# Kernel tuning notes

Measured on AMD Instinct MI355X. Metric: run time of the kernel, lower is better.

Reference implementation:

```python
import jax, jax.numpy as jnp
import numpy as np

B, S, F_IN = 8, 2048, 1024
H, SC = 512, 256
N_LAYERS = 3


def _glorot(key, shape):
    fan_in, fan_out = shape[-2], shape[-1]
    lim = float(np.sqrt(6.0 / (fan_in + fan_out)))
    return jax.random.uniform(key, shape, jnp.float32, -lim, lim)


def setup_inputs() -> dict:
    key = jax.random.key(0)
    ks = jax.random.split(key, 8)
    x = jax.random.normal(ks[0], (B, S, F_IN), jnp.float32)
    Wp = _glorot(ks[1], (F_IN, H)); bp = jnp.zeros((H,), jnp.float32)
    gcn_W = _glorot(ks[2], (N_LAYERS, H, H)); gcn_b = jnp.zeros((N_LAYERS, H), jnp.float32)
    s1_W = _glorot(ks[3], (H, SC)); s1_b = jnp.zeros((SC,), jnp.float32)
    s2_W = _glorot(ks[4], (SC, SC // 2)); s2_b = jnp.zeros((SC // 2,), jnp.float32)
    s3_W = _glorot(ks[5], (SC // 2, 1)); s3_b = jnp.zeros((1,), jnp.float32)
    return {"x": x, "Wp": Wp, "bp": bp, "gcn_W": gcn_W, "gcn_b": gcn_b,
            "s1_W": s1_W, "s1_b": s1_b, "s2_W": s2_W, "s2_b": s2_b,
            "s3_W": s3_W, "s3_b": s3_b}


def _build_adj(seq_len):
    # tridiagonal band: self + immediate temporal neighbors
    a = jnp.eye(seq_len, dtype=jnp.float32)
    a = a + jnp.eye(seq_len, k=1, dtype=jnp.float32) + jnp.eye(seq_len, k=-1, dtype=jnp.float32)
    deg = a.sum(axis=1)
    dinv = jnp.power(deg + 1e-8, -0.5)
    # D^{-1/2} A D^{-1/2}
    return dinv[:, None] * a * dinv[None, :]


def reference(x, Wp, bp, gcn_W, gcn_b, s1_W, s1_b, s2_W, s2_b, s3_W, s3_b):
    seq_len = x.shape[1]
    adj = _build_adj(seq_len)  # [S, S]
    h = jnp.einsum('bsf,fh->bsh', x, Wp) + bp  # feature projection
    for i in range(N_LAYERS):
        support = jnp.einsum('bsh,hk->bsk', h, gcn_W[i])
        h = jnp.einsum('st,btk->bsk', adj, support) + gcn_b[i]
        if i < N_LAYERS - 1:
            h = jax.nn.relu(h)  # dropout is identity in eval mode
    z = jax.nn.relu(jnp.einsum('bsh,hc->bsc', h, s1_W) + s1_b)
    z = jax.nn.relu(jnp.einsum('bsc,cd->bsd', z, s2_W) + s2_b)
    scores = jax.nn.sigmoid(jnp.einsum('bsd,do->bso', z, s3_W) + s3_b)
    return scores[..., 0]  # [B, S]
```

## Files before the change

### kernel.cpp

```cpp
#include <hip/hip_runtime.h>
#include <hip/hip_fp16.h>
#include <cstdint>
#include <cstddef>


typedef _Float16 f16;
typedef _Float16 f16x8 __attribute__((ext_vector_type(8)));
typedef float    f32x4 __attribute__((ext_vector_type(4)));

__device__ __forceinline__ void async_cp16(const void* g, void* l) {
  __builtin_amdgcn_global_load_lds((const __attribute__((address_space(1))) void*)g,
                                   (__attribute__((address_space(3))) void*)l, 16, 0, 0);
}

template<int BM, int BN, int WAVES_M, int WAVES_N, bool RELU, bool HAS_BIAS>
__global__ __launch_bounds__(256) void gemm_f16_kernel(
    const f16* __restrict__ A, const f16* __restrict__ BT,
    f16* __restrict__ C, const float* __restrict__ bias,
    int M, int N, int K)
{
  constexpr int BK = 64;
  constexpr int WM = BM / WAVES_M;
  constexpr int WN = BN / WAVES_N;
  constexpr int TM = WM / 16;
  constexpr int TN = WN / 16;
  constexpr int ITER_A = (BM * BK) / (256 * 8);
  constexpr int ITER_B = (BN * BK) / (256 * 8);

  __shared__ __align__(16) f16 sA[BM * BK];
  __shared__ __align__(16) f16 sB[BN * BK];

  const int tid  = threadIdx.x;
  const int lane = tid & 63;
  const int wave = tid >> 6;
  const int wm   = wave / WAVES_N;
  const int wn   = wave % WAVES_N;
  const int m0   = blockIdx.x * BM;
  const int n0   = blockIdx.y * BN;

  f32x4 acc[TM][TN];
#pragma unroll
  for (int i = 0; i < TM; ++i)
#pragma unroll
    for (int j = 0; j < TN; ++j)
      acc[i][j] = (f32x4){0.f, 0.f, 0.f, 0.f};

  const int quad = lane >> 4;
  const int l16  = lane & 15;

  for (int kt = 0; kt < K; kt += BK) {
    __syncthreads();
#pragma unroll
    for (int j = 0; j < ITER_A; ++j) {
      const int linear = j * 256 + tid;
      const int row = linear >> 3;
      const int q   = (linear & 7) ^ (row & 7);
      async_cp16(A + (size_t)(m0 + row) * K + kt + q * 8, &sA[linear * 8]);
    }
#pragma unroll
    for (int j = 0; j < ITER_B; ++j) {
      const int linear = j * 256 + tid;
      const int row = linear >> 3;
      const int q   = (linear & 7) ^ (row & 7);
      async_cp16(BT + (size_t)(n0 + row) * K + kt + q * 8, &sB[linear * 8]);
    }
    __syncthreads();

#pragma unroll
    for (int kk = 0; kk < 2; ++kk) {
      const int c = quad + kk * 4;
      f16x8 af[TM], bf[TN];
#pragma unroll
      for (int mi = 0; mi < TM; ++mi) {
        const int ml = wm * WM + mi * 16 + l16;
        af[mi] = *(const f16x8*)&sA[ml * 64 + ((c ^ (ml & 7)) * 8)];
      }
#pragma unroll
      for (int ni = 0; ni < TN; ++ni) {
        const int nl = wn * WN + ni * 16 + l16;
        bf[ni] = *(const f16x8*)&sB[nl * 64 + ((c ^ (nl & 7)) * 8)];
      }
#pragma unroll
      for (int mi = 0; mi < TM; ++mi)
#pragma unroll
        for (int ni = 0; ni < TN; ++ni)
          acc[mi][ni] = __builtin_amdgcn_mfma_f32_16x16x32_f16(
              af[mi], bf[ni], acc[mi][ni], 0, 0, 0);
    }
  }

#pragma unroll
  for (int ni = 0; ni < TN; ++ni) {
    const int nc = n0 + wn * WN + ni * 16 + l16;
    const float bv = HAS_BIAS ? bias[nc] : 0.0f;
#pragma unroll
    for (int mi = 0; mi < TM; ++mi) {
#pragma unroll
      for (int r = 0; r < 4; ++r) {
        const int mr = m0 + wm * WM + mi * 16 + quad * 4 + r;
        float v = acc[mi][ni][r] + bv;
        if (RELU) v = fmaxf(v, 0.0f);
        C[(size_t)mr * N + nc] = (f16)v;
      }
    }
  }
}

__global__ __launch_bounds__(256) void band_mix_kernel(
    const f16* __restrict__ sup, f16* __restrict__ h,
    const float* __restrict__ bias, int relu)
{
  const int idx = blockIdx.x * 256 + threadIdx.x;
  const int row = idx >> 6;
  const int ch  = idx & 63;
  const int s   = row & 2047;
  const float dM = 0.57735026919f;
  const float dE = 0.70710678118f;
  const float ds = (s == 0 || s == 2047) ? dE : dM;
  const size_t off = ((size_t)row << 9) + ((size_t)ch << 3);

  f16x8 self = *(const f16x8*)(sup + off);
  float o[8];
  const float cs = ds * ds;
#pragma unroll
  for (int j = 0; j < 8; ++j) o[j] = cs * (float)self[j];
  if (s > 0) {
    const float cp = ds * ((s - 1 == 0) ? dE : dM);
    f16x8 pv = *(const f16x8*)(sup + off - 512);
#pragma unroll
    for (int j = 0; j < 8; ++j) o[j] += cp * (float)pv[j];
  }
  if (s < 2047) {
    const float cn = ds * ((s + 1 == 2047) ? dE : dM);
    f16x8 nx = *(const f16x8*)(sup + off + 512);
#pragma unroll
    for (int j = 0; j < 8; ++j) o[j] += cn * (float)nx[j];
  }
  f16x8 res;
#pragma unroll
  for (int j = 0; j < 8; ++j) {
    float v = o[j] + bias[(ch << 3) + j];
    if (relu) v = fmaxf(v, 0.0f);
    res[j] = (f16)v;
  }
  *(f16x8*)(h + off) = res;
}

__global__ __launch_bounds__(256) void head_fused_kernel(
    const f16* __restrict__ h, const f16* __restrict__ S1T,
    const f16* __restrict__ S2T,
    const float* __restrict__ s1b, const float* __restrict__ s2b,
    const float* __restrict__ s3w, const float* __restrict__ s3b,
    float* __restrict__ out)
{
  __shared__ __align__(16) char smem[40960 + 64 * 264 * 2];
  f16* sA  = (f16*)smem;
  f16* sB  = (f16*)(smem + 8192);
  f16* zs  = (f16*)(smem + 40960);
  f16* z2s = (f16*)smem;
  f16* sB2 = (f16*)(smem + 17408);

  const int tid  = threadIdx.x;
  const int lane = tid & 63;
  const int wave = tid >> 6;
  const int quad = lane >> 4;
  const int l16  = lane & 15;
  const int m0   = blockIdx.x * 64;

  f32x4 acc[4][4];
#pragma unroll
  for (int i = 0; i < 4; ++i)
#pragma unroll
    for (int j = 0; j < 4; ++j) acc[i][j] = (f32x4){0.f, 0.f, 0.f, 0.f};

  for (int kt = 0; kt < 512; kt += 64) {
    __syncthreads();
#pragma unroll
    for (int j = 0; j < 2; ++j) {
      const int linear = j * 256 + tid;
      const int row = linear >> 3;
      const int q   = (linear & 7) ^ (row & 7);
      async_cp16(h + (size_t)(m0 + row) * 512 + kt + q * 8, &sA[linear * 8]);
    }
#pragma unroll
    for (int j = 0; j < 8; ++j) {
      const int linear = j * 256 + tid;
      const int row = linear >> 3;
      const int q   = (linear & 7) ^ (row & 7);
      async_cp16(S1T + (size_t)row * 512 + kt + q * 8, &sB[linear * 8]);
    }
    __syncthreads();
#pragma unroll
    for (int kk = 0; kk < 2; ++kk) {
      const int c = quad + kk * 4;
      f16x8 af[4], bf[4];
#pragma unroll
      for (int mi = 0; mi < 4; ++mi) {
        const int ml = mi * 16 + l16;
        af[mi] = *(const f16x8*)&sA[ml * 64 + ((c ^ (ml & 7)) * 8)];
      }
#pragma unroll
      for (int ni = 0; ni < 4; ++ni) {
        const int nl = wave * 64 + ni * 16 + l16;
        bf[ni] = *(const f16x8*)&sB[nl * 64 + ((c ^ (nl & 7)) * 8)];
      }
#pragma unroll
      for (int mi = 0; mi < 4; ++mi)
#pragma unroll
        for (int ni = 0; ni < 4; ++ni)
          acc[mi][ni] = __builtin_amdgcn_mfma_f32_16x16x32_f16(
              af[mi], bf[ni], acc[mi][ni], 0, 0, 0);
    }
  }
#pragma unroll
  for (int ni = 0; ni < 4; ++ni) {
    const int nc = wave * 64 + ni * 16 + l16;
    const float bv = s1b[nc];
#pragma unroll
    for (int mi = 0; mi < 4; ++mi)
#pragma unroll
      for (int r = 0; r < 4; ++r) {
        const int row = mi * 16 + quad * 4 + r;
        zs[row * 264 + nc] = (f16)fmaxf(acc[mi][ni][r] + bv, 0.0f);
      }
  }
  __syncthreads();

  f32x4 acc2[4][2];
#pragma unroll
  for (int i = 0; i < 4; ++i)
#pragma unroll
    for (int j = 0; j < 2; ++j) acc2[i][j] = (f32x4){0.f, 0.f, 0.f, 0.f};

  for (int kt2 = 0; kt2 < 4; ++kt2) {
    __syncthreads();
#pragma unroll
    for (int j = 0; j < 4; ++j) {
      const int linear = j * 256 + tid;
      const int row = linear >> 3;
      const int q   = (linear & 7) ^ (row & 7);
      async_cp16(S2T + (size_t)row * 256 + kt2 * 64 + q * 8, &sB2[linear * 8]);
    }
    __syncthreads();
#pragma unroll
    for (int kk = 0; kk < 2; ++kk) {
      const int c = quad + kk * 4;
      f16x8 af[4], bf[2];
#pragma unroll
      for (int mi = 0; mi < 4; ++mi) {
        const int row = mi * 16 + l16;
        af[mi] = *(const f16x8*)&zs[row * 264 + (kt2 * 8 + c) * 8];
      }
#pragma unroll
      for (int ni = 0; ni < 2; ++ni) {
        const int nl = wave * 32 + ni * 16 + l16;
        bf[ni] = *(const f16x8*)&sB2[nl * 64 + ((c ^ (nl & 7)) * 8)];
      }
#pragma unroll
      for (int mi = 0; mi < 4; ++mi)
#pragma unroll
        for (int ni = 0; ni < 2; ++ni)
          acc2[mi][ni] = __builtin_amdgcn_mfma_f32_16x16x32_f16(
              af[mi], bf[ni], acc2[mi][ni], 0, 0, 0);
    }
  }
  __syncthreads();
#pragma unroll
  for (int ni = 0; ni < 2; ++ni) {
    const int nc = wave * 32 + ni * 16 + l16;
    const float bv = s2b[nc];
#pragma unroll
    for (int mi = 0; mi < 4; ++mi)
#pragma unroll
      for (int r = 0; r < 4; ++r) {
        const int row = mi * 16 + quad * 4 + r;
        z2s[row * 136 + nc] = (f16)fmaxf(acc2[mi][ni][r] + bv, 0.0f);
      }
  }
  __syncthreads();

  const int m = tid >> 2;
  const int qd = tid & 3;
  float p = 0.f;
#pragma unroll
  for (int j = 0; j < 4; ++j) {
    f16x8 v = *(const f16x8*)&z2s[m * 136 + qd * 32 + j * 8];
#pragma unroll
    for (int e = 0; e < 8; ++e) p += (float)v[e] * s3w[qd * 32 + j * 8 + e];
  }
  p += __shfl_xor(p, 1);
  p += __shfl_xor(p, 2);
  if (qd == 0) out[m0 + m] = 1.0f / (1.0f + expf(-(p + s3b[0])));
}

__global__ __launch_bounds__(256) void prep_kernel(
    const float* __restrict__ x, f16* __restrict__ xh,
    const float* __restrict__ Wp, f16* __restrict__ WpT,
    const float* __restrict__ gW, f16* __restrict__ GT,
    const float* __restrict__ s1W, f16* __restrict__ S1T,
    const float* __restrict__ s2W, f16* __restrict__ S2T)
{
  __shared__ f16 s[64 * 68];
  const int tid = threadIdx.x;
  int b = blockIdx.x;

  if (b < 8192) {
    const int i = b * 256 + tid;
    const float4* p = (const float4*)(x + ((size_t)i << 3));
    float4 a = p[0], bq = p[1];
    f16x8 o;
    o[0] = (f16)a.x;  o[1] = (f16)a.y;  o[2] = (f16)a.z;  o[3] = (f16)a.w;
    o[4] = (f16)bq.x; o[5] = (f16)bq.y; o[6] = (f16)bq.z; o[7] = (f16)bq.w;
    *(f16x8*)(xh + ((size_t)i << 3)) = o;
    return;
  }
  b -= 8192;
  const float* W; f16* WT; int K, N, tile;
  if (b < 128)      { W = Wp;  WT = WpT; K = 1024; N = 512; tile = b; }
  else if (b < 320) { const int i = (b - 128) >> 6;
                      W = gW + (size_t)i * 262144; WT = GT + (size_t)i * 262144;
                      K = 512; N = 512; tile = (b - 128) & 63; }
  else if (b < 352) { W = s1W; WT = S1T; K = 512; N = 256; tile = b - 320; }
  else              { W = s2W; WT = S2T; K = 256; N = 128; tile = b - 352; }

  const int nt = tile % (N >> 6);
  const int kt = tile / (N >> 6);
#pragma unroll
  for (int it = 0; it < 16; ++it) {
    const int i  = it * 256 + tid;
    const int rk = i >> 6, rn = i & 63;
    s[rn * 68 + rk] = (f16)W[(size_t)(kt * 64 + rk) * N + nt * 64 + rn];
  }
  __syncthreads();
#pragma unroll
  for (int it = 0; it < 16; ++it) {
    const int i  = it * 256 + tid;
    const int rn = i >> 6, rk = i & 63;
    WT[(size_t)(nt * 64 + rn) * K + kt * 64 + rk] = s[rn * 68 + rk];
  }
}

extern "C" void kernel_launch(void* const* d_in, const int* in_sizes, int n_in,
                              void* d_out, int out_size, void* d_ws, size_t ws_size,
                              hipStream_t stream) {
  (void)in_sizes; (void)n_in; (void)out_size; (void)ws_size;
  const float* x   = (const float*)d_in[0];
  const float* Wp  = (const float*)d_in[1];
  const float* bp  = (const float*)d_in[2];
  const float* gW  = (const float*)d_in[3];
  const float* gb  = (const float*)d_in[4];
  const float* s1W = (const float*)d_in[5];
  const float* s1b = (const float*)d_in[6];
  const float* s2W = (const float*)d_in[7];
  const float* s2b = (const float*)d_in[8];
  const float* s3W = (const float*)d_in[9];
  const float* s3b = (const float*)d_in[10];
  float* out = (float*)d_out;

  constexpr int M = 16384;
  char* ws = (char*)d_ws;
  f16* xh  = (f16*)(ws + 0);
  f16* sup = (f16*)(ws + 0);
  f16* h   = (f16*)(ws + 33554432);
  f16* WpT = (f16*)(ws + 50331648);
  f16* GT  = (f16*)(ws + 51380224);
  f16* S1T = (f16*)(ws + 52953088);
  f16* S2T = (f16*)(ws + 53215232);

  prep_kernel<<<8552, 256, 0, stream>>>(x, xh, Wp, WpT, gW, GT, s1W, S1T, s2W, S2T);

  gemm_f16_kernel<128, 128, 2, 2, false, true>
      <<<dim3(M / 128, 4), 256, 0, stream>>>(xh, WpT, h, bp, M, 512, 1024);

  for (int i = 0; i < 3; ++i) {
    gemm_f16_kernel<128, 128, 2, 2, false, false>
        <<<dim3(M / 128, 4), 256, 0, stream>>>(h, GT + (size_t)i * 262144, sup,
                                               nullptr, M, 512, 512);
    band_mix_kernel<<<4096, 256, 0, stream>>>(sup, h, gb + (size_t)i * 512, (i < 2) ? 1 : 0);
  }

  head_fused_kernel<<<M / 64, 256, 0, stream>>>(h, S1T, S2T, s1b, s2b, s3W, s3b, out);
}
```

Before: 233.9 us.

## Fuse fp32->fp16 cast into projection GEMM and band mixing into GCN GEMM loads

The x fp32->fp16 conversion moves into the projection GEMM's A-tile load, so the separate pass over x and the xh buffer go away. The tridiagonal adjacency mix is applied to the input rows before each GCN GEMM instead of to the outputs after it, which is valid because A(hW) = (Ah)W. This removes the band_mix kernels and their round trips through the sup buffer, with bias and ReLU moved into the GEMM epilogue. In exchange, A loads become synchronous register loads instead of async global-to-LDS copies, each GCN tile reads three neighbouring rows, and the mixing now runs in fp16 arithmetic with fp16 coefficients, which costs some precision.

```diff
diff --git a/kernel.cpp b/kernel.cpp
--- a/kernel.cpp
+++ b/kernel.cpp
@@ -13,9 +13,16 @@
                                    (__attribute__((address_space(3))) void*)l, 16, 0, 0);
 }
 
-template<int BM, int BN, int WAVES_M, int WAVES_N, bool RELU, bool HAS_BIAS>
+__device__ __forceinline__ f16x8 splat8(f16 v) {
+  f16x8 r;
+#pragma unroll
+  for (int e = 0; e < 8; ++e) r[e] = v;
+  return r;
+}
+
+template<int BM, int BN, int WAVES_M, int WAVES_N, bool RELU, bool HAS_BIAS, int AMODE>
 __global__ __launch_bounds__(256) void gemm_f16_kernel(
-    const f16* __restrict__ A, const f16* __restrict__ BT,
+    const void* __restrict__ Aptr, const f16* __restrict__ BT,
     f16* __restrict__ C, const float* __restrict__ bias,
     int M, int N, int K)
 {
@@ -26,6 +33,7 @@
   constexpr int TN = WN / 16;
   constexpr int ITER_A = (BM * BK) / (256 * 8);
   constexpr int ITER_B = (BN * BK) / (256 * 8);
+  constexpr int S = 2048;
 
   __shared__ __align__(16) f16 sA[BM * BK];
   __shared__ __align__(16) f16 sB[BN * BK];
@@ -38,6 +46,33 @@
   const int m0   = blockIdx.x * BM;
   const int n0   = blockIdx.y * BN;
 
+  uint32_t offA[ITER_A][3];
+  f16      cfA[ITER_A][3];
+  const float dM = 0.57735026919f;
+  const float dE = 0.70710678118f;
+#pragma unroll
+  for (int j = 0; j < ITER_A; ++j) {
+    const int linear = j * 256 + tid;
+    const int row = linear >> 3;
+    const int q   = (linear & 7) ^ (row & 7);
+    const int gm  = m0 + row;
+    if constexpr (AMODE == 1) {
+      offA[j][0] = (uint32_t)(((size_t)gm * K + q * 8) * 4);
+    } else {
+      const int s = gm & (S - 1);
+      const float dsv = (s == 0 || s == S - 1) ? dE : dM;
+      const float cpf = (s > 0)     ? dsv * ((s - 1 == 0) ? dE : dM)     : 0.0f;
+      const float csf = dsv * dsv;
+      const float cnf = (s < S - 1) ? dsv * ((s + 1 == S - 1) ? dE : dM) : 0.0f;
+      const int rm1 = (s > 0)     ? gm - 1 : gm;
+      const int rp1 = (s < S - 1) ? gm + 1 : gm;
+      offA[j][0] = (uint32_t)(((size_t)rm1 * K + q * 8) * 2);
+      offA[j][1] = (uint32_t)(((size_t)gm  * K + q * 8) * 2);
+      offA[j][2] = (uint32_t)(((size_t)rp1 * K + q * 8) * 2);
+      cfA[j][0] = (f16)cpf; cfA[j][1] = (f16)csf; cfA[j][2] = (f16)cnf;
+    }
+  }
+
   f32x4 acc[TM][TN];
 #pragma unroll
   for (int i = 0; i < TM; ++i)
@@ -50,12 +85,29 @@
 
   for (int kt = 0; kt < K; kt += BK) {
     __syncthreads();
-#pragma unroll
-    for (int j = 0; j < ITER_A; ++j) {
-      const int linear = j * 256 + tid;
-      const int row = linear >> 3;
-      const int q   = (linear & 7) ^ (row & 7);
-      async_cp16(A + (size_t)(m0 + row) * K + kt + q * 8, &sA[linear * 8]);
+    if constexpr (AMODE == 1) {
+      const char* base = (const char*)Aptr + (size_t)kt * 4;
+#pragma unroll
+      for (int j = 0; j < ITER_A; ++j) {
+        const float4* p = (const float4*)(base + offA[j][0]);
+        const float4 a = p[0], b = p[1];
+        f16x8 o;
+        o[0] = (f16)a.x;  o[1] = (f16)a.y;  o[2] = (f16)a.z;  o[3] = (f16)a.w;
+        o[4] = (f16)b.x;  o[5] = (f16)b.y;  o[6] = (f16)b.z;  o[7] = (f16)b.w;
+        *(f16x8*)&sA[(size_t)(j * 256 + tid) * 8] = o;
+      }
+    } else {
+      const char* base = (const char*)Aptr + (size_t)kt * 2;
+#pragma unroll
+      for (int j = 0; j < ITER_A; ++j) {
+        f16x8 pv = *(const f16x8*)(base + offA[j][0]);
+        f16x8 sv = *(const f16x8*)(base + offA[j][1]);
+        f16x8 nv = *(const f16x8*)(base + offA[j][2]);
+        f16x8 r = pv * splat8(cfA[j][0]);
+        r += sv * splat8(cfA[j][1]);
+        r += nv * splat8(cfA[j][2]);
+        *(f16x8*)&sA[(size_t)(j * 256 + tid) * 8] = r;
+      }
     }
 #pragma unroll
     for (int j = 0; j < ITER_B; ++j) {
@@ -104,46 +156,6 @@
       }
     }
   }
-}
-
-__global__ __launch_bounds__(256) void band_mix_kernel(
-    const f16* __restrict__ sup, f16* __restrict__ h,
-    const float* __restrict__ bias, int relu)
-{
-  const int idx = blockIdx.x * 256 + threadIdx.x;
-  const int row = idx >> 6;
-  const int ch  = idx & 63;
-  const int s   = row & 2047;
-  const float dM = 0.57735026919f;
-  const float dE = 0.70710678118f;
-  const float ds = (s == 0 || s == 2047) ? dE : dM;
-  const size_t off = ((size_t)row << 9) + ((size_t)ch << 3);
-
-  f16x8 self = *(const f16x8*)(sup + off);
-  float o[8];
-  const float cs = ds * ds;
-#pragma unroll
-  for (int j = 0; j < 8; ++j) o[j] = cs * (float)self[j];
-  if (s > 0) {
-    const float cp = ds * ((s - 1 == 0) ? dE : dM);
-    f16x8 pv = *(const f16x8*)(sup + off - 512);
-#pragma unroll
-    for (int j = 0; j < 8; ++j) o[j] += cp * (float)pv[j];
-  }
-  if (s < 2047) {
-    const float cn = ds * ((s + 1 == 2047) ? dE : dM);
-    f16x8 nx = *(const f16x8*)(sup + off + 512);
-#pragma unroll
-    for (int j = 0; j < 8; ++j) o[j] += cn * (float)nx[j];
-  }
-  f16x8 res;
-#pragma unroll
-  for (int j = 0; j < 8; ++j) {
-    float v = o[j] + bias[(ch << 3) + j];
-    if (relu) v = fmaxf(v, 0.0f);
-    res[j] = (f16)v;
-  }
-  *(f16x8*)(h + off) = res;
 }
 
 __global__ __launch_bounds__(256) void head_fused_kernel(
@@ -294,7 +306,6 @@
 }
 
 __global__ __launch_bounds__(256) void prep_kernel(
-    const float* __restrict__ x, f16* __restrict__ xh,
     const float* __restrict__ Wp, f16* __restrict__ WpT,
     const float* __restrict__ gW, f16* __restrict__ GT,
     const float* __restrict__ s1W, f16* __restrict__ S1T,
@@ -304,17 +315,6 @@
   const int tid = threadIdx.x;
   int b = blockIdx.x;
 
-  if (b < 8192) {
-    const int i = b * 256 + tid;
-    const float4* p = (const float4*)(x + ((size_t)i << 3));
-    float4 a = p[0], bq = p[1];
-    f16x8 o;
-    o[0] = (f16)a.x;  o[1] = (f16)a.y;  o[2] = (f16)a.z;  o[3] = (f16)a.w;
-    o[4] = (f16)bq.x; o[5] = (f16)bq.y; o[6] = (f16)bq.z; o[7] = (f16)bq.w;
-    *(f16x8*)(xh + ((size_t)i << 3)) = o;
-    return;
-  }
-  b -= 8192;
   const float* W; f16* WT; int K, N, tile;
   if (b < 128)      { W = Wp;  WT = WpT; K = 1024; N = 512; tile = b; }
   else if (b < 320) { const int i = (b - 128) >> 6;
@@ -359,25 +359,24 @@
 
   constexpr int M = 16384;
   char* ws = (char*)d_ws;
-  f16* xh  = (f16*)(ws + 0);
-  f16* sup = (f16*)(ws + 0);
-  f16* h   = (f16*)(ws + 33554432);
-  f16* WpT = (f16*)(ws + 50331648);
-  f16* GT  = (f16*)(ws + 51380224);
-  f16* S1T = (f16*)(ws + 52953088);
-  f16* S2T = (f16*)(ws + 53215232);
-
-  prep_kernel<<<8552, 256, 0, stream>>>(x, xh, Wp, WpT, gW, GT, s1W, S1T, s2W, S2T);
-
-  gemm_f16_kernel<128, 128, 2, 2, false, true>
-      <<<dim3(M / 128, 4), 256, 0, stream>>>(xh, WpT, h, bp, M, 512, 1024);
-
-  for (int i = 0; i < 3; ++i) {
-    gemm_f16_kernel<128, 128, 2, 2, false, false>
-        <<<dim3(M / 128, 4), 256, 0, stream>>>(h, GT + (size_t)i * 262144, sup,
-                                               nullptr, M, 512, 512);
-    band_mix_kernel<<<4096, 256, 0, stream>>>(sup, h, gb + (size_t)i * 512, (i < 2) ? 1 : 0);
-  }
-
-  head_fused_kernel<<<M / 64, 256, 0, stream>>>(h, S1T, S2T, s1b, s2b, s3W, s3b, out);
-}
+  f16* hA  = (f16*)(ws + 0);
+  f16* hB  = (f16*)(ws + 16777216);
+  f16* WpT = (f16*)(ws + 33554432);
+  f16* GT  = (f16*)(ws + 34603008);
+  f16* S1T = (f16*)(ws + 36175872);
+  f16* S2T = (f16*)(ws + 36438016);
+
+  prep_kernel<<<360, 256, 0, stream>>>(Wp, WpT, gW, GT, s1W, S1T, s2W, S2T);
+
+  gemm_f16_kernel<128, 128, 2, 2, false, true, 1>
+      <<<dim3(M / 128, 4), 256, 0, stream>>>(x, WpT, hA, bp, M, 512, 1024);
+
+  gemm_f16_kernel<128, 128, 2, 2, true, true, 2>
+      <<<dim3(M / 128, 4), 256, 0, stream>>>(hA, GT, hB, gb, M, 512, 512);
+  gemm_f16_kernel<128, 128, 2, 2, true, true, 2>
+      <<<dim3(M / 128, 4), 256, 0, stream>>>(hB, GT + 262144, hA, gb + 512, M, 512, 512);
+  gemm_f16_kernel<128, 128, 2, 2, false, true, 2>
+      <<<dim3(M / 128, 4), 256, 0, stream>>>(hA, GT + 524288, hB, gb + 1024, M, 512, 512);
+
+  head_fused_kernel<<<M / 64, 256, 0, stream>>>(hB, S1T, S2T, s1b, s2b, s3W, s3b, out);
+}
```

Measured after the change: 235.9 us. No clear change (+0.9%).
